# Kernel tuning notes

Hardware: AMD Instinct MI355X
Metric: run time of the kernel (lower is better)

Reference implementation:

```python
import jax, jax.numpy as jnp
import numpy as np


def _lap(cost):
    """Jonker-Volgenant / e-maxx O(n^3) Hungarian (min-cost) on a square
    float64 cost matrix. Returns col index assigned to each row, matching
    scipy.optimize.linear_sum_assignment for square inputs.
    Inner column scan is vectorized with numpy.
    """
    n = cost.shape[0]
    INF = np.inf
    C = np.zeros((n + 1, n + 1), dtype=np.float64)
    C[1:, 1:] = cost  # 1-indexed
    u = np.zeros(n + 1)
    v = np.zeros(n + 1)
    p = np.zeros(n + 1, dtype=np.int64)    # p[j] = row matched to col j
    way = np.zeros(n + 1, dtype=np.int64)
    for i in range(1, n + 1):
        p[0] = i
        j0 = 0
        minv = np.full(n + 1, INF)
        used = np.zeros(n + 1, dtype=bool)
        while True:
            used[j0] = True
            i0 = p[j0]
            free = ~used
            free[0] = False
            cur = C[i0] - u[i0] - v
            upd = free & (cur < minv)
            minv = np.where(upd, cur, minv)
            way[upd] = j0
            mv = np.where(free, minv, INF)
            j1 = int(np.argmin(mv))
            delta = mv[j1]
            u[p[used]] += delta
            v[used] -= delta
            minv = np.where(free, minv - delta, minv)
            j0 = j1
            if p[j0] == 0:
                break
        # augment along alternating path
        while j0 != 0:
            j1 = way[j0]
            p[j0] = p[j1]
            j0 = j1
    col_for_row = np.zeros(n, dtype=np.int64)
    col_for_row[p[1:] - 1] = np.arange(n)
    return col_for_row


def _match(D_np):
    """Per-sample min-max normalize (detached) then Hungarian match."""
    B, N, _ = D_np.shape
    cols = np.zeros((B, N), dtype=np.int64)
    for b in range(B):
        Db = D_np[b]
        d_min = Db.min()
        d_range = Db.max() - d_min + 1e-8
        cols[b] = _lap((Db - d_min) / d_range)
    return cols


def setup_inputs() -> dict:
    key = jax.random.key(0)
    B, N = 32, 512
    D = jax.random.uniform(key, (B, N, N), dtype=jnp.float32)
    return {"D": D}


def reference(D):
    B, N, _ = D.shape
    # Matching indices are computed on detached, normalized costs (CPU, like
    # the original .cpu().numpy() round-trip).
    D_np = np.asarray(jax.device_get(D), dtype=np.float64)
    cols = jnp.asarray(_match(D_np))                      # [B, N]
    bi = jnp.arange(B)[:, None]
    ri = jnp.arange(N)[None, :]
    matched = D[bi, ri, cols]                             # [B, N], original D
    return matched.mean(axis=1).mean()
```

## Files before the change

### kernel.cpp

```cpp
#include <hip/hip_runtime.h>
#include <hip/hip_fp16.h>


#define NN 512
#define LPT 8
#define BIGF 1e30f
#define QCAP 2080
#define ARRCAP 1536
#define TOTAL_BLOCKS 256

#define DPP_MINF(x, CTRL) do {                                                  \
    float _t = __int_as_float(__builtin_amdgcn_update_dpp(                      \
        __float_as_int(x), __float_as_int(x), CTRL, 0xf, 0xf, false));          \
    (x) = _t < (x) ? _t : (x);                                                  \
} while (0)

__device__ __forceinline__ float wave_min_f32(float x) {
    DPP_MINF(x, 0x111);
    DPP_MINF(x, 0x112);
    DPP_MINF(x, 0x114);
    DPP_MINF(x, 0x118);
    DPP_MINF(x, 0x142);
    DPP_MINF(x, 0x143);
    return __int_as_float(__builtin_amdgcn_readlane(__float_as_int(x), 63));
}

__device__ __forceinline__ void wavebar() { __builtin_amdgcn_wave_barrier(); }

__device__ __forceinline__ int sel8i(const int a[LPT], int slot) {
    int r = a[0];
    #pragma unroll
    for (int s = 1; s < LPT; ++s) r = (slot == s) ? a[s] : r;
    return r;
}
__device__ __forceinline__ float sel8f(const float a[LPT], int slot) {
    float r = a[0];
    #pragma unroll
    for (int s = 1; s < LPT; ++s) r = (slot == s) ? a[s] : r;
    return r;
}
__device__ __forceinline__ void argmin8(const float e[LPT], float& bv, int& bs) {
    float v01 = e[1] < e[0] ? e[1] : e[0]; int s01 = e[1] < e[0] ? 1 : 0;
    float v23 = e[3] < e[2] ? e[3] : e[2]; int s23 = e[3] < e[2] ? 3 : 2;
    float v45 = e[5] < e[4] ? e[5] : e[4]; int s45 = e[5] < e[4] ? 5 : 4;
    float v67 = e[7] < e[6] ? e[7] : e[6]; int s67 = e[7] < e[6] ? 7 : 6;
    float v03 = v23 < v01 ? v23 : v01;     int s03 = v23 < v01 ? s23 : s01;
    float v47 = v67 < v45 ? v67 : v45;     int s47 = v67 < v45 ? s67 : s45;
    bv = v47 < v03 ? v47 : v03;            bs = v47 < v03 ? s47 : s03;
}

__global__ void zero_kernel(int* __restrict__ done) {
    if (threadIdx.x == 0) *done = 0;
}

template <bool F16>
__global__ __launch_bounds__(64)
void hungarian_kernel(const float* __restrict__ D, const __half* __restrict__ Hm,
                      double* __restrict__ bsum, int* __restrict__ done, int B) {
    const int b    = blockIdx.x;
    const int lane = threadIdx.x;

    if (b >= B) {
        const unsigned long long t0 = __builtin_amdgcn_s_memrealtime();
        float x = 1.0f + (float)lane * 1e-6f;
        while (true) {
            #pragma unroll
            for (int k = 0; k < 512; ++k) x = __builtin_fmaf(x, 1.0000001f, 1e-9f);
            if (__hip_atomic_load(done, __ATOMIC_RELAXED, __HIP_MEMORY_SCOPE_AGENT) >= B)
                break;
            if (__builtin_amdgcn_s_memrealtime() - t0 > 1200000ull)
                break;
        }
        if (x == -1.0f) bsum[B] = (double)x;
        return;
    }

    const float*  __restrict__ Db = D + (size_t)b * NN * NN;
    const __half* __restrict__ Hb = F16 ? (Hm + (size_t)b * NN * NN) : (const __half*)nullptr;

    __shared__ __align__(16) int pc[NN];
    __shared__ __align__(16) int wayc[NN];
    __shared__ __align__(16) int xrowc[NN];
    __shared__ int q[QCAP];
    __shared__ int qn;

    for (int k = lane; k < NN; k += 64) { pc[k] = 0; wayc[k] = 0; xrowc[k] = 0; }
    wavebar();

    const int col0 = lane * LPT;

    auto loadrow = [&](int r, float rv[LPT]) {
        if constexpr (F16) {
            const uint4 qv = *(const uint4*)(Hb + (size_t)(r - 1) * NN + col0);
            __half2 h0 = *(__half2*)&qv.x, h1 = *(__half2*)&qv.y,
                    h2 = *(__half2*)&qv.z, h3 = *(__half2*)&qv.w;
            float2 f0 = __half22float2(h0), f1 = __half22float2(h1),
                   f2 = __half22float2(h2), f3 = __half22float2(h3);
            rv[0]=f0.x; rv[1]=f0.y; rv[2]=f1.x; rv[3]=f1.y;
            rv[4]=f2.x; rv[5]=f2.y; rv[6]=f3.x; rv[7]=f3.y;
        } else {
            const float4* rp = (const float4*)(Db + (size_t)(r - 1) * NN + col0);
            const float4 a = rp[0], c = rp[1];
            rv[0]=a.x; rv[1]=a.y; rv[2]=a.z; rv[3]=a.w;
            rv[4]=c.x; rv[5]=c.y; rv[6]=c.z; rv[7]=c.w;
        }
    };
    auto loadsc = [&](int r, int j) -> float {
        if constexpr (F16) return __half2float(Hb[(size_t)(r - 1) * NN + (j - 1)]);
        else               return Db[(size_t)(r - 1) * NN + (j - 1)];
    };

    float v[LPT];
    int   preg[LPT];

    {
        float cmin[LPT]; int cidx[LPT];
        #pragma unroll
        for (int s = 0; s < LPT; ++s) { cmin[s] = BIGF; cidx[s] = 0; }
        #pragma unroll 4
        for (int r = 1; r <= NN; ++r) {
            float rv[LPT]; loadrow(r, rv);
            #pragma unroll
            for (int s = 0; s < LPT; ++s) {
                const bool c = rv[s] < cmin[s];
                cidx[s] = c ? r : cidx[s];
                cmin[s] = c ? rv[s] : cmin[s];
            }
        }
        #pragma unroll
        for (int s = 0; s < LPT; ++s) v[s] = cmin[s];
        *(int4*)&wayc[col0]     = make_int4(cidx[0], cidx[1], cidx[2], cidx[3]);
        *(int4*)&wayc[col0 + 4] = make_int4(cidx[4], cidx[5], cidx[6], cidx[7]);
        wavebar();
        if (lane == 0) {
            for (int j = NN; j >= 1; --j) {
                const int i = wayc[j - 1];
                if (xrowc[i - 1] == 0) { xrowc[i - 1] = j; pc[j - 1] = i; }
            }
        }
        wavebar();
        const int4 p0 = *(const int4*)&pc[col0];
        const int4 p1 = *(const int4*)&pc[col0 + 4];
        preg[0]=p0.x; preg[1]=p0.y; preg[2]=p0.z; preg[3]=p0.w;
        preg[4]=p1.x; preg[5]=p1.y; preg[6]=p1.z; preg[7]=p1.w;
    }

    int xr[LPT];
    {
        const int4 x0 = *(const int4*)&xrowc[col0];
        const int4 x1 = *(const int4*)&xrowc[col0 + 4];
        xr[0]=x0.x; xr[1]=x0.y; xr[2]=x0.z; xr[3]=x0.w;
        xr[4]=x1.x; xr[5]=x1.y; xr[6]=x1.z; xr[7]=x1.w;
    }

    for (int i = 1; i <= NN; ++i) {
        const int jx = __builtin_amdgcn_readlane(sel8i(xr, (i - 1) & 7), (i - 1) >> 3);
        if (jx == 0) continue;
        float rv[LPT]; loadrow(i, rv);
        const int  ow = (jx - 1) >> 3, sl = (jx - 1) & 7;
        const bool am = (lane == ow);
        float lm = BIGF;
        #pragma unroll
        for (int s = 0; s < LPT; ++s) {
            const float t = (am && s == sl) ? BIGF : (rv[s] - v[s]);
            lm = t < lm ? t : lm;
        }
        const float mu = wave_min_f32(lm);
        #pragma unroll
        for (int s = 0; s < LPT; ++s)
            if (am && s == sl) v[s] = rv[s] - mu;
    }

    if (lane == 0) {
        int t = 0;
        for (int r = 1; r <= NN; ++r) if (xrowc[r - 1] == 0) q[t++] = r;
        qn = t;
    }
    wavebar();
    {
        int tail = qn, head = 0, processed = 0;
        while (head < tail && processed < ARRCAP) {
            const int i = q[head]; ++head; ++processed;
            float rv[LPT]; loadrow(i, rv);
            float cur[LPT];
            #pragma unroll
            for (int s = 0; s < LPT; ++s) cur[s] = rv[s] - v[s];
            float b1; int bs1; argmin8(cur, b1, bs1);
            const float u1 = wave_min_f32(b1);
            const unsigned long long m1 = __ballot(b1 == u1);
            const int owner = __ffsll(m1) - 1;
            const int j1    = __builtin_amdgcn_readlane(col0 + bs1 + 1, owner);
            const int slotU = (j1 - 1) & 7;
            const bool am   = (lane == owner);
            #pragma unroll
            for (int s = 0; s < LPT; ++s)
                if (am && s == slotU) cur[s] = BIGF;
            float b2 = BIGF;
            #pragma unroll
            for (int s = 0; s < LPT; ++s) b2 = cur[s] < b2 ? cur[s] : b2;
            const float u2 = wave_min_f32(b2);
            const int  i1  = __builtin_amdgcn_readlane(sel8i(preg, slotU), owner);
            const bool steal  = (u1 < u2);
            const bool assign = (i1 == 0) || (steal && (tail < QCAP - 1));
            if (assign) {
                #pragma unroll
                for (int s = 0; s < LPT; ++s) {
                    if (am && s == slotU) {
                        if (steal) v[s] -= (u2 - u1);
                        preg[s] = i;
                    }
                }
                if (lane == 0) {
                    pc[j1 - 1] = i; xrowc[i - 1] = j1;
                    if (i1) { xrowc[i1 - 1] = 0; q[tail] = i1; }
                }
                if (i1) ++tail;
            }
            wavebar();
        }
    }
    wavebar();

    if (lane == 0) {
        int t = 0;
        for (int r = 1; r <= NN; ++r) if (xrowc[r - 1] == 0) q[t++] = r;
        qn = t;
    }
    wavebar();
    const int nfree = qn;

    for (int fi = 0; fi < nfree; ++fi) {
        const int rootI = q[fi];

        float minv[LPT], blk[LPT], w[LPT];
        int   wayreg[LPT];
        #pragma unroll
        for (int s = 0; s < LPT; ++s) { minv[s] = BIGF; blk[s] = 0.0f; wayreg[s] = 0; }
        float uu = 0.0f;
        int   j0 = 0;

        float rv[LPT]; loadrow(rootI, rv);
        #pragma unroll
        for (int s = 0; s < LPT; ++s) w[s] = rv[s] - v[s];

        int j1; float dmin;
        while (true) {
            #pragma unroll
            for (int s = 0; s < LPT; ++s) {
                const float c  = (w[s] - uu) + blk[s];
                const bool upd = c < minv[s];
                wayreg[s] = upd ? j0 : wayreg[s];
                minv[s]   = upd ? c  : minv[s];
            }
            float e[LPT];
            #pragma unroll
            for (int s = 0; s < LPT; ++s) e[s] = minv[s] + blk[s];
            float bv; int bs; argmin8(e, bv, bs);
            dmin = wave_min_f32(bv);
            const unsigned long long mk = __ballot(bv == dmin);
            const int owner = __ffsll(mk) - 1;
            j1 = __builtin_amdgcn_readlane(col0 + bs + 1, owner);
            const int slotU = (j1 - 1) & 7;
            const int i0n   = __builtin_amdgcn_readlane(sel8i(preg, slotU), owner);
            if (i0n == 0) break;

            const float csc = loadsc(i0n, j1);
            loadrow(i0n, rv);
            const float vj1 = __int_as_float(__builtin_amdgcn_readlane(
                __float_as_int(sel8f(v, slotU)), owner));
            const bool am = (lane == owner);
            #pragma unroll
            for (int s = 0; s < LPT; ++s)
                if (am && s == slotU) blk[s] = BIGF;
            uu = csc - vj1 - dmin;
            #pragma unroll
            for (int s = 0; s < LPT; ++s) w[s] = rv[s] - v[s];
            j0 = j1;
        }
        const float dfinal = dmin;
        j0 = j1;

        #pragma unroll
        for (int s = 0; s < LPT; ++s)
            if (blk[s] == BIGF) v[s] += minv[s] - dfinal;
        *(int4*)&wayc[col0]     = make_int4(wayreg[0], wayreg[1], wayreg[2], wayreg[3]);
        *(int4*)&wayc[col0 + 4] = make_int4(wayreg[4], wayreg[5], wayreg[6], wayreg[7]);
        wavebar();
        if (lane == 0) {
            int jj = j0;
            while (jj != 0) {
                const int jp = wayc[jj - 1];
                pc[jj - 1] = jp ? pc[jp - 1] : rootI;
                jj = jp;
            }
        }
        wavebar();
        const int4 p0 = *(const int4*)&pc[col0];
        const int4 p1 = *(const int4*)&pc[col0 + 4];
        preg[0]=p0.x; preg[1]=p0.y; preg[2]=p0.z; preg[3]=p0.w;
        preg[4]=p1.x; preg[5]=p1.y; preg[6]=p1.z; preg[7]=p1.w;
    }

    double acc = 0.0;
    #pragma unroll
    for (int s = 0; s < LPT; ++s) {
        const int r = preg[s];
        acc += (double)Db[(size_t)(r - 1) * NN + (col0 + s)];
    }
    #pragma unroll
    for (int m = 1; m < 64; m <<= 1) acc += __shfl_xor(acc, m, 64);
    if (lane == 0) {
        bsum[b] = acc;
        __threadfence();
        atomicAdd(done, 1);
    }
}

__global__ void cvt_kernel(const float* __restrict__ D, __half* __restrict__ H, int n4) {
    const int idx = blockIdx.x * blockDim.x + threadIdx.x;
    const int stride = gridDim.x * blockDim.x;
    const float4* __restrict__ D4 = (const float4*)D;
    __half2* __restrict__ H2 = (__half2*)H;
    for (int i = idx; i < n4; i += stride) {
        const float4 f = D4[i];
        H2[2 * i]     = __floats2half2_rn(f.x, f.y);
        H2[2 * i + 1] = __floats2half2_rn(f.z, f.w);
    }
}

__global__ void finalize_kernel(const double* __restrict__ bsum, float* __restrict__ out, int B) {
    if (threadIdx.x == 0 && blockIdx.x == 0) {
        double acc = 0.0;
        for (int b = 0; b < B; ++b) acc += bsum[b] / (double)NN;
        out[0] = (float)(acc / (double)B);
    }
}

extern "C" void kernel_launch(void* const* d_in, const int* in_sizes, int n_in,
                              void* d_out, int out_size, void* d_ws, size_t ws_size,
                              hipStream_t stream) {
    (void)n_in; (void)out_size;
    const float* D    = (const float*)d_in[0];
    float*       out  = (float*)d_out;
    int*         done = (int*)d_ws;
    double*      bsum = (double*)((char*)d_ws + 64);

    const int B = in_sizes[0] / (NN * NN);
    const size_t need = 512 + (size_t)B * NN * NN * sizeof(__half);

    zero_kernel<<<1, 64, 0, stream>>>(done);
    if (ws_size >= need) {
        __half* Hm = (__half*)((char*)d_ws + 512);
        const int n4 = (B * NN * NN) / 4;
        cvt_kernel<<<1024, 256, 0, stream>>>(D, Hm, n4);
        hungarian_kernel<true><<<dim3(TOTAL_BLOCKS), dim3(64), 0, stream>>>(D, Hm, bsum, done, B);
    } else {
        hungarian_kernel<false><<<dim3(TOTAL_BLOCKS), dim3(64), 0, stream>>>(D, nullptr, bsum, done, B);
    }
    finalize_kernel<<<1, 64, 0, stream>>>(bsum, out, B);
}
```

Baseline: 2.905 ms.

## Prefetch speculative next rows in Hungarian reduction, ARR, and augmentation loops

Software-pipelines row loads in three phases. The row-reduction loop double-buffers rows. The auction/ARR queue prefetches the next queued row. The Dijkstra augmentation loop speculatively guesses the next column from minv before the current row's update, then prefetches that row, its cost entry and v. When the guess matches the actual next column, the loaded data is reused, hiding global-memory latency on the serial dependency chain. This costs extra argmin reductions and loads on misses, adds register pressure, and lowers the filler-block timeout.

```diff
diff --git a/kernel.cpp b/kernel.cpp
--- a/kernel.cpp
+++ b/kernel.cpp
@@ -68,7 +68,7 @@
             for (int k = 0; k < 512; ++k) x = __builtin_fmaf(x, 1.0000001f, 1e-9f);
             if (__hip_atomic_load(done, __ATOMIC_RELAXED, __HIP_MEMORY_SCOPE_AGENT) >= B)
                 break;
-            if (__builtin_amdgcn_s_memrealtime() - t0 > 1200000ull)
+            if (__builtin_amdgcn_s_memrealtime() - t0 > 800000ull)
                 break;
         }
         if (x == -1.0f) bsum[B] = (double)x;
@@ -153,22 +153,31 @@
         xr[4]=x1.x; xr[5]=x1.y; xr[6]=x1.z; xr[7]=x1.w;
     }
 
-    for (int i = 1; i <= NN; ++i) {
-        const int jx = __builtin_amdgcn_readlane(sel8i(xr, (i - 1) & 7), (i - 1) >> 3);
-        if (jx == 0) continue;
-        float rv[LPT]; loadrow(i, rv);
-        const int  ow = (jx - 1) >> 3, sl = (jx - 1) & 7;
-        const bool am = (lane == ow);
-        float lm = BIGF;
-        #pragma unroll
-        for (int s = 0; s < LPT; ++s) {
-            const float t = (am && s == sl) ? BIGF : (rv[s] - v[s]);
-            lm = t < lm ? t : lm;
-        }
-        const float mu = wave_min_f32(lm);
-        #pragma unroll
-        for (int s = 0; s < LPT; ++s)
-            if (am && s == sl) v[s] = rv[s] - mu;
+    {
+        auto rt_process = [&](int i, const float rv[LPT]) {
+            const int jx = __builtin_amdgcn_readlane(sel8i(xr, (i - 1) & 7), (i - 1) >> 3);
+            if (jx == 0) return;
+            const int  ow = (jx - 1) >> 3, sl = (jx - 1) & 7;
+            const bool am = (lane == ow);
+            float lm = BIGF;
+            #pragma unroll
+            for (int s = 0; s < LPT; ++s) {
+                const float t = (am && s == sl) ? BIGF : (rv[s] - v[s]);
+                lm = t < lm ? t : lm;
+            }
+            const float mu = wave_min_f32(lm);
+            #pragma unroll
+            for (int s = 0; s < LPT; ++s)
+                if (am && s == sl) v[s] = rv[s] - mu;
+        };
+        float bufA[LPT], bufB[LPT];
+        loadrow(1, bufA);
+        for (int i = 1; i <= NN; i += 2) {
+            if (i + 1 <= NN) loadrow(i + 1, bufB);
+            rt_process(i, bufA);
+            if (i + 2 <= NN) loadrow(i + 2, bufA);
+            if (i + 1 <= NN) rt_process(i + 1, bufB);
+        }
     }
 
     if (lane == 0) {
@@ -179,9 +188,19 @@
     wavebar();
     {
         int tail = qn, head = 0, processed = 0;
+        int pfi = 0; float pfrow[LPT];
+        if (head < tail) { pfi = q[head]; loadrow(pfi, pfrow); }
         while (head < tail && processed < ARRCAP) {
             const int i = q[head]; ++head; ++processed;
-            float rv[LPT]; loadrow(i, rv);
+            float rv[LPT];
+            if (i == pfi) {
+                #pragma unroll
+                for (int s = 0; s < LPT; ++s) rv[s] = pfrow[s];
+            } else {
+                loadrow(i, rv);
+            }
+            if (head < tail) { pfi = q[head]; loadrow(pfi, pfrow); } else pfi = 0;
+
             float cur[LPT];
             #pragma unroll
             for (int s = 0; s < LPT; ++s) cur[s] = rv[s] - v[s];
@@ -239,55 +258,90 @@
         float uu = 0.0f;
         int   j0 = 0;
 
-        float rv[LPT]; loadrow(rootI, rv);
+        int   sj2 = -1, si2 = 0;
+        float svj2 = 0.0f, scsc = 0.0f, srow[LPT];
         #pragma unroll
-        for (int s = 0; s < LPT; ++s) w[s] = rv[s] - v[s];
-
-        int j1; float dmin;
+        for (int s = 0; s < LPT; ++s) srow[s] = 0.0f;
+
+        {
+            float rv[LPT]; loadrow(rootI, rv);
+            #pragma unroll
+            for (int s = 0; s < LPT; ++s) w[s] = rv[s] - v[s];
+        }
+
+        int j1fin; float dfinal;
         while (true) {
+            float e[LPT];
             #pragma unroll
             for (int s = 0; s < LPT; ++s) {
                 const float c  = (w[s] - uu) + blk[s];
                 const bool upd = c < minv[s];
                 wayreg[s] = upd ? j0 : wayreg[s];
                 minv[s]   = upd ? c  : minv[s];
-            }
-            float e[LPT];
-            #pragma unroll
-            for (int s = 0; s < LPT; ++s) e[s] = minv[s] + blk[s];
+                e[s]      = minv[s] + blk[s];
+            }
             float bv; int bs; argmin8(e, bv, bs);
-            dmin = wave_min_f32(bv);
+            const float dmin = wave_min_f32(bv);
             const unsigned long long mk = __ballot(bv == dmin);
             const int owner = __ffsll(mk) - 1;
-            j1 = __builtin_amdgcn_readlane(col0 + bs + 1, owner);
+            const int j1    = __builtin_amdgcn_readlane(col0 + bs + 1, owner);
             const int slotU = (j1 - 1) & 7;
-            const int i0n   = __builtin_amdgcn_readlane(sel8i(preg, slotU), owner);
-            if (i0n == 0) break;
-
-            const float csc = loadsc(i0n, j1);
-            loadrow(i0n, rv);
-            const float vj1 = __int_as_float(__builtin_amdgcn_readlane(
-                __float_as_int(sel8f(v, slotU)), owner));
+
+            const bool hit = (j1 == sj2);
+            const int  i0n = hit ? si2
+                                 : __builtin_amdgcn_readlane(sel8i(preg, slotU), owner);
+            if (i0n == 0) { j1fin = j1; dfinal = dmin; break; }
+
+            float csc, vj1;
+            if (hit) {
+                csc = scsc; vj1 = svj2;
+                #pragma unroll
+                for (int s = 0; s < LPT; ++s) w[s] = srow[s] - v[s];
+            } else {
+                csc = loadsc(i0n, j1);
+                float rvn[LPT]; loadrow(i0n, rvn);
+                vj1 = __int_as_float(__builtin_amdgcn_readlane(
+                    __float_as_int(sel8f(v, slotU)), owner));
+                #pragma unroll
+                for (int s = 0; s < LPT; ++s) w[s] = rvn[s] - v[s];
+            }
+            uu = csc - vj1 - dmin;
+
             const bool am = (lane == owner);
             #pragma unroll
             for (int s = 0; s < LPT; ++s)
                 if (am && s == slotU) blk[s] = BIGF;
-            uu = csc - vj1 - dmin;
-            #pragma unroll
-            for (int s = 0; s < LPT; ++s) w[s] = rv[s] - v[s];
             j0 = j1;
-        }
-        const float dfinal = dmin;
-        j0 = j1;
+
+            float e2[LPT];
+            #pragma unroll
+            for (int s = 0; s < LPT; ++s) e2[s] = minv[s] + blk[s];
+            float bv2; int bs2; argmin8(e2, bv2, bs2);
+            const float d2 = wave_min_f32(bv2);
+            const unsigned long long mk2 = __ballot(bv2 == d2);
+            const int owner2 = __ffsll(mk2) - 1;
+            const int j2     = __builtin_amdgcn_readlane(col0 + bs2 + 1, owner2);
+            const int slot2  = (j2 - 1) & 7;
+            si2  = __builtin_amdgcn_readlane(sel8i(preg, slot2), owner2);
+            svj2 = __int_as_float(__builtin_amdgcn_readlane(
+                __float_as_int(sel8f(v, slot2)), owner2));
+            sj2  = j2;
+            if (si2 > 0) {
+                scsc = loadsc(si2, j2);
+                loadrow(si2, srow);
+            }
+        }
+        const float dfin = dfinal;
+        int j0a = j1fin;
 
         #pragma unroll
         for (int s = 0; s < LPT; ++s)
-            if (blk[s] == BIGF) v[s] += minv[s] - dfinal;
+            if (blk[s] == BIGF) v[s] += minv[s] - dfin;
         *(int4*)&wayc[col0]     = make_int4(wayreg[0], wayreg[1], wayreg[2], wayreg[3]);
         *(int4*)&wayc[col0 + 4] = make_int4(wayreg[4], wayreg[5], wayreg[6], wayreg[7]);
         wavebar();
         if (lane == 0) {
-            int jj = j0;
+            int jj = j0a;
             while (jj != 0) {
                 const int jp = wayc[jj - 1];
                 pc[jj - 1] = jp ? pc[jp - 1] : rootI;
```

Result: slower. 3.782 ms (+30.2%).
